# Performance work log

Hardware: AMD Instinct MI355X
Metric: run time of the kernel (lower is better)

Reference implementation:

```python
import jax, jax.numpy as jnp
import numpy as np

N_NODES = 100000
D_IN = 256
D_HID = 64
D_EMB = 32
ADJ_NNZ = 3200000
N_EDGES = 2000000


def setup_inputs() -> dict:
    key = jax.random.key(0)
    ks = jax.random.split(key, 8)
    x = jax.random.normal(ks[0], (N_NODES, D_IN), dtype=jnp.float32)
    adj_src = jax.random.randint(ks[1], (ADJ_NNZ,), 0, N_NODES, dtype=jnp.int32)
    adj_dst = jax.random.randint(ks[2], (ADJ_NNZ,), 0, N_NODES, dtype=jnp.int32)
    adj_val = jax.random.uniform(ks[3], (ADJ_NNZ,), dtype=jnp.float32)
    edge_index = jax.random.randint(ks[4], (2, N_EDGES), 0, N_NODES, dtype=jnp.int32)
    # Xavier-uniform weights, zero biases (matches reset_parameters)
    lim1 = float(np.sqrt(6.0 / (D_IN + D_HID)))
    lim2 = float(np.sqrt(6.0 / (D_HID + D_EMB)))
    W1 = jax.random.uniform(ks[5], (D_IN, D_HID), minval=-lim1, maxval=lim1, dtype=jnp.float32)
    b1 = jnp.zeros((D_HID,), dtype=jnp.float32)
    W2 = jax.random.uniform(ks[6], (D_HID, D_EMB), minval=-lim2, maxval=lim2, dtype=jnp.float32)
    b2 = jnp.zeros((D_EMB,), dtype=jnp.float32)
    return {"x": x, "adj_src": adj_src, "adj_dst": adj_dst, "adj_val": adj_val,
            "edge_index": edge_index, "W1": W1, "b1": b1, "W2": W2, "b2": b2}


def _spmm(adj_src, adj_dst, adj_val, dense):
    # (sparse A) @ dense : out[i] = sum_{e: dst[e]==i} val[e] * dense[src[e]]
    n = dense.shape[0]
    msgs = adj_val[:, None] * dense[adj_src]            # [nnz, d]
    return jax.ops.segment_sum(msgs, adj_dst, num_segments=n)


def reference(x, adj_src, adj_dst, adj_val, edge_index, W1, b1, W2, b2):
    # Layer 1: ReLU(A_norm @ (x W1) + b1)
    z1 = jax.nn.relu(_spmm(adj_src, adj_dst, adj_val, x @ W1) + b1)
    # Layer 2: A_norm @ (z1 W2) + b2 (no activation)
    z2 = _spmm(adj_src, adj_dst, adj_val, z1 @ W2) + b2   # [n, d_emb]
    # Inner-product decoder over edges
    src, dst = edge_index[0], edge_index[1]
    scores = jnp.sum(z2[src] * z2[dst], axis=1)          # [num_edges]
    return scores
```

## Files before the change

kernel.cpp:

```cpp
#include <hip/hip_runtime.h>
#include <hip/hip_bf16.h>


#define D_IN  256
#define D_HID 64
#define D_EMB 32
#define BROWS 256
#define NBUK_MAX 512
#define TILE  4096
#define PBS   512
#define SBS   1024

typedef unsigned char u8;
typedef unsigned short u16;
typedef unsigned int u32;
typedef __attribute__((ext_vector_type(8))) short short8;
typedef __attribute__((ext_vector_type(4))) float f32x4;
typedef __attribute__((ext_vector_type(2))) float f32x2;

__device__ __forceinline__ float bf2f(u32 u) {
  return __uint_as_float((u & 0xFFFFu) << 16);
}
__device__ __forceinline__ float bf2f_hi(u32 u) {
  return __uint_as_float(u & 0xFFFF0000u);
}
__device__ __forceinline__ u16 f2bf(float f) {
  u32 x = __float_as_uint(f);
  x += 0x7FFFu + ((x >> 16) & 1u);
  return (u16)(x >> 16);
}
__device__ __forceinline__ u32 cvtpk_bf16(float lo, float hi) {
  u32 r;
  asm("v_cvt_pk_bf16_f32 %0, %1, %2" : "=v"(r) : "v"(lo), "v"(hi));
  return r;
}
__device__ __forceinline__ void unpack8(uint4 u, float* f) {
  f[0] = bf2f(u.x); f[1] = bf2f(u.x >> 16);
  f[2] = bf2f(u.y); f[3] = bf2f(u.y >> 16);
  f[4] = bf2f(u.z); f[5] = bf2f(u.z >> 16);
  f[6] = bf2f(u.w); f[7] = bf2f(u.w >> 16);
}

__global__ __launch_bounds__(256) void w1_swizzle_kernel(
    const float* __restrict__ W1, uint4* __restrict__ gswz) {
  const int s = blockIdx.x * 256 + threadIdx.x;
  const int lane = s & 63;
  const int kstep = (s >> 6) & 7;
  const int nt = s >> 9;
  const int col = nt * 16 + (lane & 15);
  const int kbase = kstep * 32 + (lane >> 4) * 8;
  u32 p[4];
  for (int jp = 0; jp < 4; ++jp) {
    u32 lo = f2bf(W1[(kbase + 2 * jp) * D_HID + col]);
    u32 hi = f2bf(W1[(kbase + 2 * jp + 1) * D_HID + col]);
    p[jp] = lo | (hi << 16);
  }
  gswz[s] = make_uint4(p[0], p[1], p[2], p[3]);
}

__global__ __launch_bounds__(256) void bin_count(
    const int* __restrict__ dst, int* __restrict__ hist, int nnz, int nbuk) {
  __shared__ int h[NBUK_MAX];
  for (int i = threadIdx.x; i < nbuk; i += 256) h[i] = 0;
  __syncthreads();
  const int stride = gridDim.x * 256;
  for (int e = blockIdx.x * 256 + threadIdx.x; e < nnz; e += stride)
    atomicAdd(&h[dst[e] >> 8], 1);
  __syncthreads();
  for (int i = threadIdx.x; i < nbuk; i += 256) {
    int v = h[i];
    if (v) atomicAdd(&hist[i], v);
  }
}

__global__ __launch_bounds__(256) void bin_scan(
    int* __restrict__ hist, int* __restrict__ cur, int n) {
  __shared__ int sm[256];
  const int t = threadIdx.x;
  const int per = (n + 255) / 256;
  const int base = t * per;
  int loc[4];
  int s = 0;
  for (int i = 0; i < per; ++i) {
    int idx = base + i;
    int v = (idx < n) ? hist[idx] : 0;
    loc[i] = s;
    s += v;
  }
  sm[t] = s;
  __syncthreads();
  for (int off = 1; off < 256; off <<= 1) {
    int tmp = (t >= off) ? sm[t - off] : 0;
    __syncthreads();
    sm[t] += tmp;
    __syncthreads();
  }
  const int b0 = sm[t] - s;
  for (int i = 0; i < per; ++i) {
    int idx = base + i;
    if (idx < n) {
      int p = b0 + loc[i];
      hist[idx] = p;
      cur[idx] = p;
    }
  }
  if (t == 255) hist[n] = sm[255];
}

__global__ __launch_bounds__(PBS) void partition_kernel(
    const int* __restrict__ src, const int* __restrict__ dst,
    const float* __restrict__ val, int* __restrict__ cur,
    int2* __restrict__ payload, int nnz, int nbuk) {
  __shared__ int2 stage[TILE];
  __shared__ int hist[NBUK_MAX];
  __shared__ int lcur[NBUK_MAX];
  __shared__ int gbase[NBUK_MAX];
  __shared__ int sm[PBS];

  const int t = threadIdx.x;
  const long long base = (long long)blockIdx.x * TILE;
  const int cnt = min(TILE, (int)(nnz - base));

  for (int i = t; i < nbuk; i += PBS) hist[i] = 0;
  __syncthreads();

  constexpr int PER = TILE / PBS;
  int key[PER], vq[PER];
  short bk[PER];
  for (int i = 0; i < PER; ++i) {
    int idx = t + i * PBS;
    if (idx < cnt) {
      int d = dst[base + idx];
      int b = d >> 8;
      bk[i] = (short)b;
      key[i] = (src[base + idx] << 8) | (d & (BROWS - 1));
      int q = (int)(val[base + idx] * 32768.f + 0.5f);
      q = min(q, 32767);
      vq[i] = (b << 15) | q;
      atomicAdd(&hist[b], 1);
    } else {
      bk[i] = -1;
    }
  }
  __syncthreads();

  {
    int c = (t < nbuk) ? hist[t] : 0;
    sm[t] = c;
    __syncthreads();
    for (int off = 1; off < PBS; off <<= 1) {
      int tmp = (t >= off) ? sm[t - off] : 0;
      __syncthreads();
      sm[t] += tmp;
      __syncthreads();
    }
    int excl = sm[t] - c;
    if (t < nbuk) {
      hist[t] = excl;
      lcur[t] = excl;
      if (c > 0) gbase[t] = atomicAdd(&cur[t], c);
    }
  }
  __syncthreads();

  for (int i = 0; i < PER; ++i) {
    if (bk[i] >= 0) {
      int p = atomicAdd(&lcur[bk[i]], 1);
      stage[p] = make_int2(key[i], vq[i]);
    }
  }
  __syncthreads();

  for (int i = t; i < cnt; i += PBS) {
    int2 pk = stage[i];
    int b = pk.y >> 15;
    payload[gbase[b] + (i - hist[b])] = pk;
  }
}

__global__ __launch_bounds__(SBS) void bucket_sort_kernel(
    const int* __restrict__ bscan, const int2* __restrict__ payload,
    u32* __restrict__ csr, int* __restrict__ rs, int M) {
  __shared__ int cnt_s[BROWS];
  __shared__ int sm[BROWS];
  const int b = blockIdx.x;
  const int t = threadIdx.x;
  const int start = bscan[b];
  const int end = bscan[b + 1];

  if (t < BROWS) cnt_s[t] = 0;
  __syncthreads();
  for (int j = start + t; j < end; j += SBS)
    atomicAdd(&cnt_s[payload[j].x & (BROWS - 1)], 1);
  __syncthreads();

  int v = 0;
  if (t < BROWS) { v = cnt_s[t]; sm[t] = v; }
  __syncthreads();
  for (int off = 1; off < BROWS; off <<= 1) {
    int tmp = 0;
    if (t < BROWS && t >= off) tmp = sm[t - off];
    __syncthreads();
    if (t < BROWS) sm[t] += tmp;
    __syncthreads();
  }
  if (t < BROWS) {
    int row = b * BROWS + t;
    if (row < M) rs[row] = start + sm[t];
    cnt_s[t] = start + sm[t] - v;
  }
  __syncthreads();

  for (int j = start + t; j < end; j += SBS) {
    int2 pk = payload[j];
    int r = pk.x & (BROWS - 1);
    int p = atomicAdd(&cnt_s[r], 1);
    csr[p] = ((u32)(pk.x >> 8) << 15) | (u32)(pk.y & 32767);
  }
}

__global__ __launch_bounds__(256) void gemm1_mfma_kernel(
    const float* __restrict__ x, const uint4* __restrict__ gswz,
    u8* __restrict__ h1, int M) {
  const int tid = threadIdx.x;
  const int wv = tid >> 6;
  const int lane = tid & 63;
  const int quad = lane >> 4;
  const int m = lane & 15;

  const int rowbase = blockIdx.x * 64 + wv * 16;
  int arow = rowbase + m;
  if (arow >= M) arow = M - 1;

  f32x4 acc[4];
  for (int nt = 0; nt < 4; ++nt) acc[nt] = (f32x4){0.f, 0.f, 0.f, 0.f};

  const float* xrow = &x[(long long)arow * D_IN];

#pragma unroll
  for (int kstep = 0; kstep < 8; ++kstep) {
    const int kbase = kstep * 32 + quad * 8;
    float4 a0 = *(const float4*)&xrow[kbase];
    float4 a1 = *(const float4*)&xrow[kbase + 4];
    uint4 au;
    au.x = cvtpk_bf16(a0.x, a0.y);
    au.y = cvtpk_bf16(a0.z, a0.w);
    au.z = cvtpk_bf16(a1.x, a1.y);
    au.w = cvtpk_bf16(a1.z, a1.w);
    short8 af = *(short8*)&au;
#pragma unroll
    for (int nt = 0; nt < 4; ++nt) {
      uint4 bu = gswz[(nt * 8 + kstep) * 64 + lane];
      short8 bf = *(short8*)&bu;
      acc[nt] = __builtin_amdgcn_mfma_f32_16x16x32_bf16(af, bf, acc[nt], 0, 0, 0);
    }
  }

#pragma unroll
  for (int nt = 0; nt < 4; ++nt) {
#pragma unroll
    for (int r = 0; r < 4; ++r) {
      int orow = rowbase + quad * 4 + r;
      if (orow < M) {
        int pk8 = __builtin_amdgcn_cvt_pk_fp8_f32(acc[nt][r], 0.f, 0, false);
        h1[(u32)orow * D_HID + nt * 16 + m] = (u8)(pk8 & 0xFF);
      }
    }
  }
}

__global__ __launch_bounds__(256) void spmm1_gemm2_fused(
    const int* __restrict__ rs, const u32* __restrict__ csr,
    const u8* __restrict__ in, const float* __restrict__ b1,
    const float* __restrict__ W2, u16* __restrict__ h2, int M) {
  __shared__ float w2s[D_HID * D_EMB];
  __shared__ float z1s[16][68];

  const int tid = threadIdx.x;
  for (int i = tid; i < D_HID * D_EMB / 4; i += 256)
    ((float4*)w2s)[i] = ((const float4*)W2)[i];
  __syncthreads();

  const int lt = tid & 15;
  const int tb = tid >> 4;
  const int row = blockIdx.x * 16 + tb;
  if (row >= M) return;

  const int start = (row == 0) ? 0 : rs[row - 1];
  const int end = rs[row];
  const float qs = 1.f / 32768.f;
  const u8* inp = in + lt * 4;

  float a0 = 0.f, a1 = 0.f, a2 = 0.f, a3 = 0.f;
  int j = start;

#define GATHER_FMA(PK)                                                \
  {                                                                   \
    u32 wq = *(const u32*)(inp + (((PK) >> 15) << 6));                \
    float v = (float)((PK) & 32767u) * qs;                            \
    f32x2 lo = __builtin_amdgcn_cvt_pk_f32_fp8(wq, false);            \
    f32x2 hi = __builtin_amdgcn_cvt_pk_f32_fp8(wq, true);             \
    a0 = fmaf(v, lo.x, a0); a1 = fmaf(v, lo.y, a1);                   \
    a2 = fmaf(v, hi.x, a2); a3 = fmaf(v, hi.y, a3);                   \
  }

  int head = (4 - (start & 3)) & 3;
  if (head > end - start) head = end - start;
  for (int h = 0; h < head; ++h, ++j) {
    u32 pk = csr[j];
    GATHER_FMA(pk);
  }

  for (; j + 8 <= end; j += 8) {
    uint4 pa = *(const uint4*)&csr[j];
    uint4 pb = *(const uint4*)&csr[j + 4];
    u32 w0 = *(const u32*)(inp + ((pa.x >> 15) << 6));
    u32 w1 = *(const u32*)(inp + ((pa.y >> 15) << 6));
    u32 w2 = *(const u32*)(inp + ((pa.z >> 15) << 6));
    u32 w3 = *(const u32*)(inp + ((pa.w >> 15) << 6));
    u32 w4 = *(const u32*)(inp + ((pb.x >> 15) << 6));
    u32 w5 = *(const u32*)(inp + ((pb.y >> 15) << 6));
    u32 w6 = *(const u32*)(inp + ((pb.z >> 15) << 6));
    u32 w7 = *(const u32*)(inp + ((pb.w >> 15) << 6));
    float v0 = (float)(pa.x & 32767u) * qs;
    float v1 = (float)(pa.y & 32767u) * qs;
    float v2 = (float)(pa.z & 32767u) * qs;
    float v3 = (float)(pa.w & 32767u) * qs;
    float v4 = (float)(pb.x & 32767u) * qs;
    float v5 = (float)(pb.y & 32767u) * qs;
    float v6 = (float)(pb.z & 32767u) * qs;
    float v7 = (float)(pb.w & 32767u) * qs;
    f32x2 l0 = __builtin_amdgcn_cvt_pk_f32_fp8(w0, false);
    f32x2 h0 = __builtin_amdgcn_cvt_pk_f32_fp8(w0, true);
    f32x2 l1 = __builtin_amdgcn_cvt_pk_f32_fp8(w1, false);
    f32x2 h1f = __builtin_amdgcn_cvt_pk_f32_fp8(w1, true);
    f32x2 l2 = __builtin_amdgcn_cvt_pk_f32_fp8(w2, false);
    f32x2 h2f = __builtin_amdgcn_cvt_pk_f32_fp8(w2, true);
    f32x2 l3 = __builtin_amdgcn_cvt_pk_f32_fp8(w3, false);
    f32x2 h3 = __builtin_amdgcn_cvt_pk_f32_fp8(w3, true);
    f32x2 l4 = __builtin_amdgcn_cvt_pk_f32_fp8(w4, false);
    f32x2 h4 = __builtin_amdgcn_cvt_pk_f32_fp8(w4, true);
    f32x2 l5 = __builtin_amdgcn_cvt_pk_f32_fp8(w5, false);
    f32x2 h5 = __builtin_amdgcn_cvt_pk_f32_fp8(w5, true);
    f32x2 l6 = __builtin_amdgcn_cvt_pk_f32_fp8(w6, false);
    f32x2 h6 = __builtin_amdgcn_cvt_pk_f32_fp8(w6, true);
    f32x2 l7 = __builtin_amdgcn_cvt_pk_f32_fp8(w7, false);
    f32x2 h7 = __builtin_amdgcn_cvt_pk_f32_fp8(w7, true);
    a0 = fmaf(v0, l0.x, a0); a1 = fmaf(v0, l0.y, a1);
    a2 = fmaf(v0, h0.x, a2); a3 = fmaf(v0, h0.y, a3);
    a0 = fmaf(v1, l1.x, a0); a1 = fmaf(v1, l1.y, a1);
    a2 = fmaf(v1, h1f.x, a2); a3 = fmaf(v1, h1f.y, a3);
    a0 = fmaf(v2, l2.x, a0); a1 = fmaf(v2, l2.y, a1);
    a2 = fmaf(v2, h2f.x, a2); a3 = fmaf(v2, h2f.y, a3);
    a0 = fmaf(v3, l3.x, a0); a1 = fmaf(v3, l3.y, a1);
    a2 = fmaf(v3, h3.x, a2); a3 = fmaf(v3, h3.y, a3);
    a0 = fmaf(v4, l4.x, a0); a1 = fmaf(v4, l4.y, a1);
    a2 = fmaf(v4, h4.x, a2); a3 = fmaf(v4, h4.y, a3);
    a0 = fmaf(v5, l5.x, a0); a1 = fmaf(v5, l5.y, a1);
    a2 = fmaf(v5, h5.x, a2); a3 = fmaf(v5, h5.y, a3);
    a0 = fmaf(v6, l6.x, a0); a1 = fmaf(v6, l6.y, a1);
    a2 = fmaf(v6, h6.x, a2); a3 = fmaf(v6, h6.y, a3);
    a0 = fmaf(v7, l7.x, a0); a1 = fmaf(v7, l7.y, a1);
    a2 = fmaf(v7, h7.x, a2); a3 = fmaf(v7, h7.y, a3);
  }

  for (; j < end; ++j) {
    u32 pk = csr[j];
    GATHER_FMA(pk);
  }
#undef GATHER_FMA

  const float4 bv = *(const float4*)&b1[lt * 4];
  a0 = fmaxf(a0 + bv.x, 0.f);
  a1 = fmaxf(a1 + bv.y, 0.f);
  a2 = fmaxf(a2 + bv.z, 0.f);
  a3 = fmaxf(a3 + bv.w, 0.f);

  float* zrow = z1s[tb];
  zrow[lt * 4 + 0] = a0;
  zrow[lt * 4 + 1] = a1;
  zrow[lt * 4 + 2] = a2;
  zrow[lt * 4 + 3] = a3;
  float o0 = 0.f, o1 = 0.f;
#pragma unroll
  for (int k = 0; k < D_HID; k += 4) {
    float4 z4 = *(const float4*)&zrow[k];
    o0 = fmaf(z4.x, w2s[(k + 0) * D_EMB + 2 * lt], o0);
    o1 = fmaf(z4.x, w2s[(k + 0) * D_EMB + 2 * lt + 1], o1);
    o0 = fmaf(z4.y, w2s[(k + 1) * D_EMB + 2 * lt], o0);
    o1 = fmaf(z4.y, w2s[(k + 1) * D_EMB + 2 * lt + 1], o1);
    o0 = fmaf(z4.z, w2s[(k + 2) * D_EMB + 2 * lt], o0);
    o1 = fmaf(z4.z, w2s[(k + 2) * D_EMB + 2 * lt + 1], o1);
    o0 = fmaf(z4.w, w2s[(k + 3) * D_EMB + 2 * lt], o0);
    o1 = fmaf(z4.w, w2s[(k + 3) * D_EMB + 2 * lt + 1], o1);
  }
  ((u32*)h2)[((u32)row << 4) + lt] = cvtpk_bf16(o0, o1);
}

template <int D, bool RELU>
__global__ __launch_bounds__(256) void spmm_csr_kernel(
    const int* __restrict__ rs, const u32* __restrict__ csr,
    const u16* __restrict__ in, const float* __restrict__ bias,
    u16* __restrict__ out, int M) {
  constexpr int TEAM = D / 4;
  constexpr int SH = (D == 64) ? 6 : 5;
  const int lt = threadIdx.x % TEAM;
  const int row = blockIdx.x * (256 / TEAM) + threadIdx.x / TEAM;
  if (row >= M) return;
  const int start = (row == 0) ? 0 : rs[row - 1];
  const int end = rs[row];
  const float qs = 1.f / 32768.f;
  const u16* inp = in + lt * 4;

  float a0 = 0.f, a1 = 0.f, a2 = 0.f, a3 = 0.f;
  int j = start;

  int head = (4 - (start & 3)) & 3;
  if (head > end - start) head = end - start;
  for (int h = 0; h < head; ++h, ++j) {
    u32 pk = csr[j];
    uint2 w = *(const uint2*)(inp + ((pk >> 15) << SH));
    float v = (float)(pk & 32767u) * qs;
    a0 = fmaf(v, bf2f(w.x), a0); a1 = fmaf(v, bf2f_hi(w.x), a1);
    a2 = fmaf(v, bf2f(w.y), a2); a3 = fmaf(v, bf2f_hi(w.y), a3);
  }

  for (; j + 8 <= end; j += 8) {
    uint4 pa = *(const uint4*)&csr[j];
    uint4 pb = *(const uint4*)&csr[j + 4];
    uint2 w0 = *(const uint2*)(inp + ((pa.x >> 15) << SH));
    uint2 w1 = *(const uint2*)(inp + ((pa.y >> 15) << SH));
    uint2 w2 = *(const uint2*)(inp + ((pa.z >> 15) << SH));
    uint2 w3 = *(const uint2*)(inp + ((pa.w >> 15) << SH));
    uint2 w4 = *(const uint2*)(inp + ((pb.x >> 15) << SH));
    uint2 w5 = *(const uint2*)(inp + ((pb.y >> 15) << SH));
    uint2 w6 = *(const uint2*)(inp + ((pb.z >> 15) << SH));
    uint2 w7 = *(const uint2*)(inp + ((pb.w >> 15) << SH));
    float v0 = (float)(pa.x & 32767u) * qs;
    float v1 = (float)(pa.y & 32767u) * qs;
    float v2 = (float)(pa.z & 32767u) * qs;
    float v3 = (float)(pa.w & 32767u) * qs;
    float v4 = (float)(pb.x & 32767u) * qs;
    float v5 = (float)(pb.y & 32767u) * qs;
    float v6 = (float)(pb.z & 32767u) * qs;
    float v7 = (float)(pb.w & 32767u) * qs;
    a0 = fmaf(v0, bf2f(w0.x), a0); a1 = fmaf(v0, bf2f_hi(w0.x), a1);
    a2 = fmaf(v0, bf2f(w0.y), a2); a3 = fmaf(v0, bf2f_hi(w0.y), a3);
    a0 = fmaf(v1, bf2f(w1.x), a0); a1 = fmaf(v1, bf2f_hi(w1.x), a1);
    a2 = fmaf(v1, bf2f(w1.y), a2); a3 = fmaf(v1, bf2f_hi(w1.y), a3);
    a0 = fmaf(v2, bf2f(w2.x), a0); a1 = fmaf(v2, bf2f_hi(w2.x), a1);
    a2 = fmaf(v2, bf2f(w2.y), a2); a3 = fmaf(v2, bf2f_hi(w2.y), a3);
    a0 = fmaf(v3, bf2f(w3.x), a0); a1 = fmaf(v3, bf2f_hi(w3.x), a1);
    a2 = fmaf(v3, bf2f(w3.y), a2); a3 = fmaf(v3, bf2f_hi(w3.y), a3);
    a0 = fmaf(v4, bf2f(w4.x), a0); a1 = fmaf(v4, bf2f_hi(w4.x), a1);
    a2 = fmaf(v4, bf2f(w4.y), a2); a3 = fmaf(v4, bf2f_hi(w4.y), a3);
    a0 = fmaf(v5, bf2f(w5.x), a0); a1 = fmaf(v5, bf2f_hi(w5.x), a1);
    a2 = fmaf(v5, bf2f(w5.y), a2); a3 = fmaf(v5, bf2f_hi(w5.y), a3);
    a0 = fmaf(v6, bf2f(w6.x), a0); a1 = fmaf(v6, bf2f_hi(w6.x), a1);
    a2 = fmaf(v6, bf2f(w6.y), a2); a3 = fmaf(v6, bf2f_hi(w6.y), a3);
    a0 = fmaf(v7, bf2f(w7.x), a0); a1 = fmaf(v7, bf2f_hi(w7.x), a1);
    a2 = fmaf(v7, bf2f(w7.y), a2); a3 = fmaf(v7, bf2f_hi(w7.y), a3);
  }

  for (; j + 4 <= end; j += 4) {
    uint4 p = *(const uint4*)&csr[j];
    uint2 w0 = *(const uint2*)(inp + ((p.x >> 15) << SH));
    uint2 w1 = *(const uint2*)(inp + ((p.y >> 15) << SH));
    uint2 w2 = *(const uint2*)(inp + ((p.z >> 15) << SH));
    uint2 w3 = *(const uint2*)(inp + ((p.w >> 15) << SH));
    float v0 = (float)(p.x & 32767u) * qs;
    float v1 = (float)(p.y & 32767u) * qs;
    float v2 = (float)(p.z & 32767u) * qs;
    float v3 = (float)(p.w & 32767u) * qs;
    a0 = fmaf(v0, bf2f(w0.x), a0); a1 = fmaf(v0, bf2f_hi(w0.x), a1);
    a2 = fmaf(v0, bf2f(w0.y), a2); a3 = fmaf(v0, bf2f_hi(w0.y), a3);
    a0 = fmaf(v1, bf2f(w1.x), a0); a1 = fmaf(v1, bf2f_hi(w1.x), a1);
    a2 = fmaf(v1, bf2f(w1.y), a2); a3 = fmaf(v1, bf2f_hi(w1.y), a3);
    a0 = fmaf(v2, bf2f(w2.x), a0); a1 = fmaf(v2, bf2f_hi(w2.x), a1);
    a2 = fmaf(v2, bf2f(w2.y), a2); a3 = fmaf(v2, bf2f_hi(w2.y), a3);
    a0 = fmaf(v3, bf2f(w3.x), a0); a1 = fmaf(v3, bf2f_hi(w3.x), a1);
    a2 = fmaf(v3, bf2f(w3.y), a2); a3 = fmaf(v3, bf2f_hi(w3.y), a3);
  }
  for (; j < end; ++j) {
    u32 pk = csr[j];
    uint2 w = *(const uint2*)(inp + ((pk >> 15) << SH));
    float v = (float)(pk & 32767u) * qs;
    a0 = fmaf(v, bf2f(w.x), a0); a1 = fmaf(v, bf2f_hi(w.x), a1);
    a2 = fmaf(v, bf2f(w.y), a2); a3 = fmaf(v, bf2f_hi(w.y), a3);
  }
  const float4 bv = *(const float4*)&bias[lt * 4];
  a0 += bv.x; a1 += bv.y; a2 += bv.z; a3 += bv.w;
  if (RELU) {
    a0 = fmaxf(a0, 0.f); a1 = fmaxf(a1, 0.f);
    a2 = fmaxf(a2, 0.f); a3 = fmaxf(a3, 0.f);
  }
  uint2 o;
  o.x = cvtpk_bf16(a0, a1);
  o.y = cvtpk_bf16(a2, a3);
  *(uint2*)&out[((u32)row << SH) + lt * 4] = o;
}

__global__ __launch_bounds__(256) void decode_kernel(
    const int* __restrict__ ei, const u16* __restrict__ z2,
    float* __restrict__ out, int nE) {
  const int t = blockIdx.x * 256 + threadIdx.x;
  const int e0 = t * 2;
  if (e0 >= nE) return;
  const bool two = (e0 + 1 < nE);

  const int2 ss = *(const int2*)&ei[e0];
  const int2 dd = *(const int2*)&ei[nE + e0];

  const uint4* za = (const uint4*)(z2 + ((u32)ss.x << 5));
  const uint4* zb = (const uint4*)(z2 + ((u32)dd.x << 5));
  const uint4* zc = (const uint4*)(z2 + ((u32)(two ? ss.y : ss.x) << 5));
  const uint4* zd = (const uint4*)(z2 + ((u32)(two ? dd.y : dd.x) << 5));

  uint4 A[2], B[2], C[2], Dv[2];
  A[0] = za[0]; A[1] = za[1];
  B[0] = zb[0]; B[1] = zb[1];
  C[0] = zc[0]; C[1] = zc[1];
  Dv[0] = zd[0]; Dv[1] = zd[1];
  uint4 A2[2], B2[2], C2[2], D2[2];
  A2[0] = za[2]; A2[1] = za[3];
  B2[0] = zb[2]; B2[1] = zb[3];
  C2[0] = zc[2]; C2[1] = zc[3];
  D2[0] = zd[2]; D2[1] = zd[3];

  float acc0 = 0.f, acc1 = 0.f;
  float a8[8], b8[8];
#pragma unroll
  for (int c = 0; c < 2; ++c) {
    unpack8(A[c], a8); unpack8(B[c], b8);
#pragma unroll
    for (int k = 0; k < 8; ++k) acc0 = fmaf(a8[k], b8[k], acc0);
    unpack8(A2[c], a8); unpack8(B2[c], b8);
#pragma unroll
    for (int k = 0; k < 8; ++k) acc0 = fmaf(a8[k], b8[k], acc0);
    unpack8(C[c], a8); unpack8(Dv[c], b8);
#pragma unroll
    for (int k = 0; k < 8; ++k) acc1 = fmaf(a8[k], b8[k], acc1);
    unpack8(C2[c], a8); unpack8(D2[c], b8);
#pragma unroll
    for (int k = 0; k < 8; ++k) acc1 = fmaf(a8[k], b8[k], acc1);
  }
  out[e0] = acc0;
  if (two) out[e0 + 1] = acc1;
}

extern "C" void kernel_launch(void* const* d_in, const int* in_sizes, int n_in,
                              void* d_out, int out_size, void* d_ws, size_t ws_size,
                              hipStream_t stream) {
  const float* x       = (const float*)d_in[0];
  const int*   adj_src = (const int*)d_in[1];
  const int*   adj_dst = (const int*)d_in[2];
  const float* adj_val = (const float*)d_in[3];
  const int*   ei      = (const int*)d_in[4];
  const float* W1      = (const float*)d_in[5];
  const float* b1      = (const float*)d_in[6];
  const float* W2      = (const float*)d_in[7];
  const float* b2      = (const float*)d_in[8];

  const int M   = in_sizes[0] / D_IN;
  const int nnz = in_sizes[1];
  const int nE  = in_sizes[4] / 2;

  const int NBUK = (M + BROWS - 1) / BROWS;

  char* ws = (char*)d_ws;
  u32*   csr     = (u32*)(ws);
  int2*  payload = (int2*)(ws + (size_t)nnz * 4);
  u16*   z2      = (u16*)(ws + (size_t)nnz * 12);
  u8*    h1      = (u8*)(ws + 44800ull * 1024);
  u16*   h2      = (u16*)(ws + 51200ull * 1024);
  uint4* gswz    = (uint4*)(ws + 60ull * 1024 * 1024);

  int* rs    = (int*)d_out;
  int* bscan = (int*)d_out + 112 * 1024;
  int* cur   = (int*)d_out + 120 * 1024;

  w1_swizzle_kernel<<<8, 256, 0, stream>>>(W1, gswz);

  hipMemsetAsync(bscan, 0, (size_t)(NBUK + 1) * 4, stream);
  bin_count<<<256, 256, 0, stream>>>(adj_dst, bscan, nnz, NBUK);
  bin_scan<<<1, 256, 0, stream>>>(bscan, cur, NBUK);
  partition_kernel<<<(nnz + TILE - 1) / TILE, PBS, 0, stream>>>(
      adj_src, adj_dst, adj_val, cur, payload, nnz, NBUK);

  bucket_sort_kernel<<<NBUK, SBS, 0, stream>>>(bscan, payload, csr, rs, M);

  gemm1_mfma_kernel<<<(M + 63) / 64, 256, 0, stream>>>(x, gswz, h1, M);

  spmm1_gemm2_fused<<<(M + 15) / 16, 256, 0, stream>>>(
      rs, csr, h1, b1, W2, h2, M);

  spmm_csr_kernel<D_EMB, false><<<(M + 31) / 32, 256, 0, stream>>>(
      rs, csr, h2, b2, z2, M);

  decode_kernel<<<(nE / 2 + 255) / 256, 256, 0, stream>>>(ei, z2, (float*)d_out, nE);
}
```

Baseline: 418.3 us.

## Fuse gemm1 into partition kernel with interleaved heterogeneous blocks

Merges the GEMM1 (x@W1 via MFMA) work into the partition kernel launch, interleaving partition blocks and GEMM blocks by block index so the memory-bound x read overlaps with the scatter-heavy partitioning. GEMM blocks now use 512 threads covering 128 rows each. The scan scratch array is aliased onto the stage buffer to save LDS. This removes one launch and lets the two independent stages share the GPU concurrently, at the cost of higher LDS/register footprint for the GEMM blocks.

```diff
diff --git a/kernel.cpp b/kernel.cpp
--- a/kernel.cpp
+++ b/kernel.cpp
@@ -107,19 +107,78 @@
   if (t == 255) hist[n] = sm[255];
 }
 
-__global__ __launch_bounds__(PBS) void partition_kernel(
+__global__ __launch_bounds__(PBS) void partition_gemm1_kernel(
     const int* __restrict__ src, const int* __restrict__ dst,
     const float* __restrict__ val, int* __restrict__ cur,
-    int2* __restrict__ payload, int nnz, int nbuk) {
+    int2* __restrict__ payload, int nnz, int nbuk, int P, int G,
+    const float* __restrict__ x, const uint4* __restrict__ gswz,
+    u8* __restrict__ h1, int M) {
   __shared__ int2 stage[TILE];
   __shared__ int hist[NBUK_MAX];
   __shared__ int lcur[NBUK_MAX];
   __shared__ int gbase[NBUK_MAX];
-  __shared__ int sm[PBS];
+
+  const int b = blockIdx.x;
+  const int mn = (P < G) ? P : G;
+  const int m2 = 2 * mn;
+  bool isPart;
+  int id;
+  if (b < m2) { isPart = !(b & 1); id = b >> 1; }
+  else        { isPart = (P > G);  id = mn + (b - m2); }
+
+  if (!isPart) {
+    const int tid = threadIdx.x;
+    const int wv = tid >> 6;
+    const int lane = tid & 63;
+    const int quad = lane >> 4;
+    const int m = lane & 15;
+
+    const int rowbase = id * 128 + wv * 16;
+    int arow = rowbase + m;
+    if (arow >= M) arow = M - 1;
+
+    f32x4 acc[4];
+    for (int nt = 0; nt < 4; ++nt) acc[nt] = (f32x4){0.f, 0.f, 0.f, 0.f};
+
+    const float* xrow = &x[(long long)arow * D_IN];
+
+#pragma unroll
+    for (int kstep = 0; kstep < 8; ++kstep) {
+      const int kbase = kstep * 32 + quad * 8;
+      float4 a0 = *(const float4*)&xrow[kbase];
+      float4 a1 = *(const float4*)&xrow[kbase + 4];
+      uint4 au;
+      au.x = cvtpk_bf16(a0.x, a0.y);
+      au.y = cvtpk_bf16(a0.z, a0.w);
+      au.z = cvtpk_bf16(a1.x, a1.y);
+      au.w = cvtpk_bf16(a1.z, a1.w);
+      short8 af = *(short8*)&au;
+#pragma unroll
+      for (int nt = 0; nt < 4; ++nt) {
+        uint4 bu = gswz[(nt * 8 + kstep) * 64 + lane];
+        short8 bf = *(short8*)&bu;
+        acc[nt] = __builtin_amdgcn_mfma_f32_16x16x32_bf16(af, bf, acc[nt], 0, 0, 0);
+      }
+    }
+
+#pragma unroll
+    for (int nt = 0; nt < 4; ++nt) {
+#pragma unroll
+      for (int r = 0; r < 4; ++r) {
+        int orow = rowbase + quad * 4 + r;
+        if (orow < M) {
+          int pk8 = __builtin_amdgcn_cvt_pk_fp8_f32(acc[nt][r], 0.f, 0, false);
+          h1[(u32)orow * D_HID + nt * 16 + m] = (u8)(pk8 & 0xFF);
+        }
+      }
+    }
+    return;
+  }
 
   const int t = threadIdx.x;
-  const long long base = (long long)blockIdx.x * TILE;
+  const long long base = (long long)id * TILE;
   const int cnt = min(TILE, (int)(nnz - base));
+  int* smp = (int*)stage;
 
   for (int i = t; i < nbuk; i += PBS) hist[i] = 0;
   __syncthreads();
@@ -131,13 +190,13 @@
     int idx = t + i * PBS;
     if (idx < cnt) {
       int d = dst[base + idx];
-      int b = d >> 8;
-      bk[i] = (short)b;
+      int bb = d >> 8;
+      bk[i] = (short)bb;
       key[i] = (src[base + idx] << 8) | (d & (BROWS - 1));
       int q = (int)(val[base + idx] * 32768.f + 0.5f);
       q = min(q, 32767);
-      vq[i] = (b << 15) | q;
-      atomicAdd(&hist[b], 1);
+      vq[i] = (bb << 15) | q;
+      atomicAdd(&hist[bb], 1);
     } else {
       bk[i] = -1;
     }
@@ -146,15 +205,15 @@
 
   {
     int c = (t < nbuk) ? hist[t] : 0;
-    sm[t] = c;
+    smp[t] = c;
     __syncthreads();
     for (int off = 1; off < PBS; off <<= 1) {
-      int tmp = (t >= off) ? sm[t - off] : 0;
+      int tmp = (t >= off) ? smp[t - off] : 0;
       __syncthreads();
-      sm[t] += tmp;
+      smp[t] += tmp;
       __syncthreads();
     }
-    int excl = sm[t] - c;
+    int excl = smp[t] - c;
     if (t < nbuk) {
       hist[t] = excl;
       lcur[t] = excl;
@@ -173,8 +232,8 @@
 
   for (int i = t; i < cnt; i += PBS) {
     int2 pk = stage[i];
-    int b = pk.y >> 15;
-    payload[gbase[b] + (i - hist[b])] = pk;
+    int bb = pk.y >> 15;
+    payload[gbase[bb] + (i - hist[bb])] = pk;
   }
 }
 
@@ -216,56 +275,6 @@
     int r = pk.x & (BROWS - 1);
     int p = atomicAdd(&cnt_s[r], 1);
     csr[p] = ((u32)(pk.x >> 8) << 15) | (u32)(pk.y & 32767);
-  }
-}
-
-__global__ __launch_bounds__(256) void gemm1_mfma_kernel(
-    const float* __restrict__ x, const uint4* __restrict__ gswz,
-    u8* __restrict__ h1, int M) {
-  const int tid = threadIdx.x;
-  const int wv = tid >> 6;
-  const int lane = tid & 63;
-  const int quad = lane >> 4;
-  const int m = lane & 15;
-
-  const int rowbase = blockIdx.x * 64 + wv * 16;
-  int arow = rowbase + m;
-  if (arow >= M) arow = M - 1;
-
-  f32x4 acc[4];
-  for (int nt = 0; nt < 4; ++nt) acc[nt] = (f32x4){0.f, 0.f, 0.f, 0.f};
-
-  const float* xrow = &x[(long long)arow * D_IN];
-
-#pragma unroll
-  for (int kstep = 0; kstep < 8; ++kstep) {
-    const int kbase = kstep * 32 + quad * 8;
-    float4 a0 = *(const float4*)&xrow[kbase];
-    float4 a1 = *(const float4*)&xrow[kbase + 4];
-    uint4 au;
-    au.x = cvtpk_bf16(a0.x, a0.y);
-    au.y = cvtpk_bf16(a0.z, a0.w);
-    au.z = cvtpk_bf16(a1.x, a1.y);
-    au.w = cvtpk_bf16(a1.z, a1.w);
-    short8 af = *(short8*)&au;
-#pragma unroll
-    for (int nt = 0; nt < 4; ++nt) {
-      uint4 bu = gswz[(nt * 8 + kstep) * 64 + lane];
-      short8 bf = *(short8*)&bu;
-      acc[nt] = __builtin_amdgcn_mfma_f32_16x16x32_bf16(af, bf, acc[nt], 0, 0, 0);
-    }
-  }
-
-#pragma unroll
-  for (int nt = 0; nt < 4; ++nt) {
-#pragma unroll
-    for (int r = 0; r < 4; ++r) {
-      int orow = rowbase + quad * 4 + r;
-      if (orow < M) {
-        int pk8 = __builtin_amdgcn_cvt_pk_fp8_f32(acc[nt][r], 0.f, 0, false);
-        h1[(u32)orow * D_HID + nt * 16 + m] = (u8)(pk8 & 0xFF);
-      }
-    }
   }
 }
 
@@ -584,12 +593,14 @@
   hipMemsetAsync(bscan, 0, (size_t)(NBUK + 1) * 4, stream);
   bin_count<<<256, 256, 0, stream>>>(adj_dst, bscan, nnz, NBUK);
   bin_scan<<<1, 256, 0, stream>>>(bscan, cur, NBUK);
-  partition_kernel<<<(nnz + TILE - 1) / TILE, PBS, 0, stream>>>(
-      adj_src, adj_dst, adj_val, cur, payload, nnz, NBUK);
+
+  const int P = (nnz + TILE - 1) / TILE;
+  const int G = (M + 127) / 128;
+  partition_gemm1_kernel<<<P + G, PBS, 0, stream>>>(
+      adj_src, adj_dst, adj_val, cur, payload, nnz, NBUK, P, G,
+      x, gswz, h1, M);
 
   bucket_sort_kernel<<<NBUK, SBS, 0, stream>>>(bscan, payload, csr, rs, M);
-
-  gemm1_mfma_kernel<<<(M + 63) / 64, 256, 0, stream>>>(x, gswz, h1, M);
 
   spmm1_gemm2_fused<<<(M + 15) / 16, 256, 0, stream>>>(
       rs, csr, h1, b1, W2, h2, M);
```

After: 416.3 us. Within noise of the previous version (-0.5%).
